# Kernel tuning notes

Measured on AMD Instinct MI355X. Metric: run time of the kernel, lower is better.

The kernel has to match this reference:

```python
import jax, jax.numpy as jnp
import numpy as np

B, H, W = 16, 512, 512
N_BINS = 511          # round(mean(shape)) - 1 for (512, 512)
MAX_R = 1.0           # (1 + min(shape)/max(shape)) / 2 for square image


def _bin_ids():
    # Precompute per-pixel radial shell index (replaces the list of boolean shell masks).
    frame = max(H, W)
    xx, yy = np.mgrid[:H, :W]
    ellipse = ((xx - H / 2) * 2 / frame) ** 2 + ((yy - W / 2) * 2 / frame) ** 2
    r2 = np.linspace(0.0, MAX_R, N_BINS + 1)[1:] ** 2
    # shell k = { r2[k-1] <= ellipse < r2[k] }; pixels with ellipse >= r2[-1] map to
    # overflow bin N_BINS and are dropped, exactly matching the xor'd ellipse masks.
    return jnp.asarray(np.searchsorted(r2, ellipse.ravel(), side='right').astype(np.int32))


BIN_IDS = _bin_ids()  # [H*W] int32 in [0, N_BINS]


def setup_inputs() -> dict:
    key = jax.random.key(0)
    k1, k2 = jax.random.split(key)
    return {
        "z_": jax.random.normal(k1, (B, H, W, 2), dtype=jnp.float32),
        "t_": jax.random.normal(k2, (B, H, W, 2), dtype=jnp.float32),
    }


def _shell_sums(x):
    # x: [B, H*W] -> per-shell sums [B, N_BINS+1] in a single fused segment-sum pass.
    return jax.vmap(lambda v: jax.ops.segment_sum(v, BIN_IDS, num_segments=N_BINS + 1))(x)


def reference(z_, t_):
    tc = t_[..., 0] + 1j * t_[..., 1]          # [B,H,W] complex target
    zc = z_[..., 0] + 1j * z_[..., 1]
    Ft = jnp.fft.fft2(tc, axes=(-2, -1))
    Fe = jnp.fft.fft2(zc - tc, axes=(-2, -1))
    norm_coeff = Ft.real ** 2 + Ft.imag ** 2   # |FFT(target)|^2, [B,H,W]
    errors = Fe.real ** 2 + Fe.imag ** 2       # |FFT(z - target)|^2
    es = _shell_sums(errors.reshape(B, -1))[:, :N_BINS]      # drop overflow bin
    ns = _shell_sums(norm_coeff.reshape(B, -1))[:, :N_BINS]
    nre = es / jnp.maximum(ns, 1e-8)           # per-batch, per-shell normed error
    # per_shell_loss = per-batch sum over shells; loss = mean over batch
    return jnp.mean(jnp.sum(nre, axis=1))
```

## Files before the change

kernel.cpp:

```cpp
#include <hip/hip_runtime.h>

#define HH 512
#define WW 512
#define NBATCH 16
#define NBINS 512

#define PI_F 3.14159265358979323846f

#define SW(r) ((r) ^ (((r) >> 4) & 0xF))

__device__ __forceinline__ float2 cadd(float2 a, float2 b){ return make_float2(a.x+b.x, a.y+b.y); }
__device__ __forceinline__ float2 csub(float2 a, float2 b){ return make_float2(a.x-b.x, a.y-b.y); }
__device__ __forceinline__ float2 cmul(float2 a, float2 b){
    return make_float2(a.x*b.x - a.y*b.y, a.x*b.y + a.y*b.x);
}

typedef __fp16 h2v __attribute__((ext_vector_type(2)));
__device__ __forceinline__ unsigned pack2(float2 v) {
    union { h2v h; unsigned u; } c;
    c.h = __builtin_amdgcn_cvt_pkrtz(v.x, v.y);
    return c.u;
}
__device__ __forceinline__ float2 unpack2(unsigned u) {
    union { unsigned u; __fp16 h[2]; } c; c.u = u;
    return make_float2((float)c.h[0], (float)c.h[1]);
}

__device__ __forceinline__ void dft8(const float2* a, float2* y) {
    const float s2 = 0.70710678118654752440f;
    float2 t02a = cadd(a[0], a[4]), t02s = csub(a[0], a[4]);
    float2 t13a = cadd(a[2], a[6]), t13s = csub(a[2], a[6]);
    float2 E0 = cadd(t02a, t13a);
    float2 E2 = csub(t02a, t13a);
    float2 E1 = make_float2(t02s.x + t13s.y, t02s.y - t13s.x);
    float2 E3 = make_float2(t02s.x - t13s.y, t02s.y + t13s.x);
    float2 u02a = cadd(a[1], a[5]), u02s = csub(a[1], a[5]);
    float2 u13a = cadd(a[3], a[7]), u13s = csub(a[3], a[7]);
    float2 O0 = cadd(u02a, u13a);
    float2 O2 = csub(u02a, u13a);
    float2 O1 = make_float2(u02s.x + u13s.y, u02s.y - u13s.x);
    float2 O3 = make_float2(u02s.x - u13s.y, u02s.y + u13s.x);
    float2 wO1 = make_float2(s2 * (O1.x + O1.y), s2 * (O1.y - O1.x));
    float2 wO2 = make_float2(O2.y, -O2.x);
    float2 wO3 = make_float2(s2 * (O3.y - O3.x), -s2 * (O3.x + O3.y));
    y[0] = cadd(E0, O0);  y[4] = csub(E0, O0);
    y[1] = cadd(E1, wO1); y[5] = csub(E1, wO1);
    y[2] = cadd(E2, wO2); y[6] = csub(E2, wO2);
    y[3] = cadd(E3, wO3); y[7] = csub(E3, wO3);
}

__device__ __forceinline__ void twiddle8(float base, float2* w) {
    float s1, c1, s4, c4;
    __sincosf(base, &s1, &c1);
    __sincosf(4.0f * base, &s4, &c4);
    w[0] = make_float2(1.0f, 0.0f);
    w[1] = make_float2(c1, s1);
    w[2] = cmul(w[1], w[1]);
    w[3] = cmul(w[2], w[1]);
    w[4] = make_float2(c4, s4);
    w[5] = cmul(w[4], w[1]);
    w[6] = cmul(w[4], w[2]);
    w[7] = cmul(w[4], w[3]);
}

__device__ __forceinline__ void fft512_x2(float2* rb0, float2* rb1, int lane,
                                          float2* a0, float2* a1,
                                          float2* y0, float2* y1) {
    float2 w[8], y[8];
    twiddle8(-PI_F * (float)lane * (1.0f / 256.0f), w);
    dft8(a0, y);
#pragma unroll
    for (int r = 0; r < 8; ++r) rb0[SW(8 * lane + r)] = cmul(y[r], w[r]);
    dft8(a1, y);
#pragma unroll
    for (int r = 0; r < 8; ++r) rb1[SW(8 * lane + r)] = cmul(y[r], w[r]);
    __builtin_amdgcn_wave_barrier();
#pragma unroll
    for (int u = 0; u < 8; ++u) a0[u] = rb0[SW(lane + 64 * u)];
#pragma unroll
    for (int u = 0; u < 8; ++u) a1[u] = rb1[SW(lane + 64 * u)];
    twiddle8(-PI_F * (float)(lane >> 3) * (1.0f / 32.0f), w);
    const int qb = (lane & 7) + ((lane >> 3) << 6);
    dft8(a0, y);
#pragma unroll
    for (int r = 0; r < 8; ++r) rb0[SW(qb + 8 * r)] = cmul(y[r], w[r]);
    dft8(a1, y);
#pragma unroll
    for (int r = 0; r < 8; ++r) rb1[SW(qb + 8 * r)] = cmul(y[r], w[r]);
    __builtin_amdgcn_wave_barrier();
#pragma unroll
    for (int u = 0; u < 8; ++u) a0[u] = rb0[SW(lane + 64 * u)];
#pragma unroll
    for (int u = 0; u < 8; ++u) a1[u] = rb1[SW(lane + 64 * u)];
    dft8(a0, y0);
    dft8(a1, y1);
}

__global__ __launch_bounds__(512, 4)
void row_fft_kernel(const float2* __restrict__ z, const float2* __restrict__ t,
                    unsigned* __restrict__ fieldsT) {
    __shared__ float2 buf[16 * 512];
    const int tid  = threadIdx.x;
    const int lane = tid & 63;
    const int g    = tid >> 6;
    const int bid  = blockIdx.x;
    const int hg   = bid & 31;
    const int b    = bid >> 5;
    const int hb   = hg << 4;
    const int r0   = hb | (g << 1);
    const size_t off0 = (((size_t)b * HH) + r0) << 9;
    const size_t off1 = off0 + 512;

    float2* rb0 = buf + ((g << 1) << 9);
    float2* rb1 = rb0 + 512;
    unsigned* tile = (unsigned*)buf;

#pragma unroll
    for (int f = 0; f < 2; ++f) {
        float2 a0[8], a1[8];
        if (f == 0) {
#pragma unroll
            for (int u = 0; u < 8; ++u) a0[u] = t[off0 + lane + 64 * u];
#pragma unroll
            for (int u = 0; u < 8; ++u) a1[u] = t[off1 + lane + 64 * u];
        } else {
#pragma unroll
            for (int u = 0; u < 8; ++u) {
                float2 zv = z[off0 + lane + 64 * u];
                float2 tv = t[off0 + lane + 64 * u];
                a0[u] = make_float2(zv.x - tv.x, zv.y - tv.y);
            }
#pragma unroll
            for (int u = 0; u < 8; ++u) {
                float2 zv = z[off1 + lane + 64 * u];
                float2 tv = t[off1 + lane + 64 * u];
                a1[u] = make_float2(zv.x - tv.x, zv.y - tv.y);
            }
        }
        float2 y0[8], y1[8];
        fft512_x2(rb0, rb1, lane, a0, a1, y0, y1);

        __syncthreads();
        const int rr0 = g << 1, rr1 = rr0 | 1;
#pragma unroll
        for (int r = 0; r < 8; ++r) {
            int c = lane + (r << 6);
            tile[rr0 * 516 + c] = pack2(y0[r]);
            tile[rr1 * 516 + c] = pack2(y1[r]);
        }
        __syncthreads();
        unsigned* outF = fieldsT + (((size_t)(b * 2 + f)) << 18);
#pragma unroll
        for (int k = 0; k < 4; ++k) {
            int e = tid + (k << 9);
            int c = e >> 2, q = e & 3;
            uint4 v;
            v.x = tile[(4 * q + 0) * 516 + c];
            v.y = tile[(4 * q + 1) * 516 + c];
            v.z = tile[(4 * q + 2) * 516 + c];
            v.w = tile[(4 * q + 3) * 516 + c];
            *(uint4*)(outF + (((size_t)c) << 9) + hb + (q << 2)) = v;
        }
        __syncthreads();
    }
}

__global__ __launch_bounds__(256, 4)
void col_fft_bin_kernel(const unsigned* __restrict__ fieldsT,
                        float* __restrict__ bins) {
    __shared__ float2 buf[8 * 512];
    __shared__ float hist[NBINS];
    const int tid  = threadIdx.x;
    const int lane = tid & 63;
    const int g    = tid >> 6;
    const int bid  = blockIdx.x;
    const int cg   = bid & 63;
    const int fl   = bid >> 6;
    const int f    = fl & 1;
    const int b    = fl >> 1;
    const int cA   = (cg << 3) | (g << 1);

    hist[tid] = 0.0f;
    hist[tid + 256] = 0.0f;
    __syncthreads();

    const unsigned* colA = fieldsT + ((((size_t)fl) << 9) + cA) * 512;
    const unsigned* colB = colA + 512;
    float2 a0[8], a1[8];
#pragma unroll
    for (int u = 0; u < 8; ++u) a0[u] = unpack2(colA[lane + (u << 6)]);
#pragma unroll
    for (int u = 0; u < 8; ++u) a1[u] = unpack2(colB[lane + (u << 6)]);

    float2* rb0 = buf + ((g << 1) << 9);
    float2* rb1 = rb0 + 512;
    float2 y0[8], y1[8];
    fft512_x2(rb0, rb1, lane, a0, a1, y0, y1);

    const float fcA = (float)(cA - 256)     * (1.0f / 256.0f);
    const float fcB = (float)(cA + 1 - 256) * (1.0f / 256.0f);
    const float fc2A = fcA * fcA, fc2B = fcB * fcB;
#pragma unroll
    for (int r = 0; r < 8; ++r) {
        int k = lane + (r << 6);
        float fr = (float)(k - 256) * (1.0f / 256.0f);
        float fr2 = fr * fr;
        float eA = fr2 + fc2A;
        float eB = fr2 + fc2B;
        if (eA < 1.0f) {
            int bin = (int)(sqrtf(eA) * 511.0f);
            atomicAdd(&hist[bin], y0[r].x * y0[r].x + y0[r].y * y0[r].y);
        }
        if (eB < 1.0f) {
            int bin = (int)(sqrtf(eB) * 511.0f);
            atomicAdd(&hist[bin], y1[r].x * y1[r].x + y1[r].y * y1[r].y);
        }
    }
    __syncthreads();
    float* gb = bins + ((size_t)f * NBATCH + b) * NBINS;
    atomicAdd(&gb[tid],       hist[tid]);
    atomicAdd(&gb[tid + 256], hist[tid + 256]);
}

__global__ __launch_bounds__(512)
void loss_kernel(const float* __restrict__ bins, float* __restrict__ outp) {
    __shared__ float red[512];
    const int tid = threadIdx.x;
    float acc = 0.0f;
    if (tid < 511) {
#pragma unroll 4
        for (int b = 0; b < NBATCH; ++b) {
            float ns = bins[((size_t)b) * NBINS + tid];
            float es = bins[((size_t)(NBATCH + b)) * NBINS + tid];
            acc += es / fmaxf(ns, 1e-8f);
        }
    }
    red[tid] = acc;
    __syncthreads();
    for (int s = 256; s > 0; s >>= 1) {
        if (tid < s) red[tid] += red[tid + s];
        __syncthreads();
    }
    if (tid == 0) outp[0] = red[0] * (1.0f / NBATCH);
}

extern "C" void kernel_launch(void* const* d_in, const int* in_sizes, int n_in,
                              void* d_out, int out_size, void* d_ws, size_t ws_size,
                              hipStream_t stream) {
    const float2* z = (const float2*)d_in[0];
    const float2* t = (const float2*)d_in[1];
    float* outp = (float*)d_out;

    const size_t binsBytes = (size_t)2 * NBATCH * NBINS * sizeof(float);
    float*    bins    = (float*)d_ws;
    unsigned* fieldsT = (unsigned*)((char*)d_ws + binsBytes);

    (void)hipMemsetAsync(bins, 0, binsBytes, stream);

    row_fft_kernel<<<NBATCH * 32, 512, 0, stream>>>(z, t, fieldsT);
    col_fft_bin_kernel<<<NBATCH * 2 * 64, 256, 0, stream>>>(fieldsT, bins);
    loss_kernel<<<1, 512, 0, stream>>>(bins, outp);
}
```

Before: 173.6 us.

## Interleave column pairs in transposed buffer, shrink row blocks, per-wave histograms

The row FFT kernel now uses 256-thread blocks handling 8 rows and loads t and z once up front, so t is not read twice. The intermediate transposed buffer is re-laid out so each column pair is stored interleaved. This lets the column kernel fetch both columns with a single 8-byte load per element. The column kernel replaces the shared block histogram with per-wave histograms that reuse the FFT scratch buffer, cutting atomic contention, and sums the four wave histograms before the global atomics. The tradeoff is more registers held live in the row kernel and smaller, 8-byte-granular transposed stores.

```diff
diff --git a/kernel.cpp b/kernel.cpp
--- a/kernel.cpp
+++ b/kernel.cpp
@@ -96,52 +96,54 @@
     dft8(a1, y1);
 }
 
-__global__ __launch_bounds__(512, 4)
+
+__global__ __launch_bounds__(256, 4)
 void row_fft_kernel(const float2* __restrict__ z, const float2* __restrict__ t,
                     unsigned* __restrict__ fieldsT) {
-    __shared__ float2 buf[16 * 512];
+    __shared__ float2 buf[8 * 512];
     const int tid  = threadIdx.x;
     const int lane = tid & 63;
     const int g    = tid >> 6;
     const int bid  = blockIdx.x;
-    const int hg   = bid & 31;
-    const int b    = bid >> 5;
-    const int hb   = hg << 4;
-    const int r0   = hb | (g << 1);
-    const size_t off0 = (((size_t)b * HH) + r0) << 9;
+    const int hg   = bid & 63;
+    const int b    = bid >> 6;
+    const int hb   = hg << 3;
+    const size_t off0 = (((size_t)b * HH) + hb + (g << 1)) << 9;
     const size_t off1 = off0 + 512;
+
+    float2 tv0[8], tv1[8], ev0[8], ev1[8];
+#pragma unroll
+    for (int u = 0; u < 8; ++u) tv0[u] = t[off0 + lane + 64 * u];
+#pragma unroll
+    for (int u = 0; u < 8; ++u) tv1[u] = t[off1 + lane + 64 * u];
+#pragma unroll
+    for (int u = 0; u < 8; ++u) {
+        float2 zv = z[off0 + lane + 64 * u];
+        ev0[u] = make_float2(zv.x - tv0[u].x, zv.y - tv0[u].y);
+    }
+#pragma unroll
+    for (int u = 0; u < 8; ++u) {
+        float2 zv = z[off1 + lane + 64 * u];
+        ev1[u] = make_float2(zv.x - tv1[u].x, zv.y - tv1[u].y);
+    }
 
     float2* rb0 = buf + ((g << 1) << 9);
     float2* rb1 = rb0 + 512;
     unsigned* tile = (unsigned*)buf;
+    const int rr0 = g << 1, rr1 = rr0 | 1;
 
 #pragma unroll
     for (int f = 0; f < 2; ++f) {
         float2 a0[8], a1[8];
-        if (f == 0) {
-#pragma unroll
-            for (int u = 0; u < 8; ++u) a0[u] = t[off0 + lane + 64 * u];
-#pragma unroll
-            for (int u = 0; u < 8; ++u) a1[u] = t[off1 + lane + 64 * u];
-        } else {
-#pragma unroll
-            for (int u = 0; u < 8; ++u) {
-                float2 zv = z[off0 + lane + 64 * u];
-                float2 tv = t[off0 + lane + 64 * u];
-                a0[u] = make_float2(zv.x - tv.x, zv.y - tv.y);
-            }
-#pragma unroll
-            for (int u = 0; u < 8; ++u) {
-                float2 zv = z[off1 + lane + 64 * u];
-                float2 tv = t[off1 + lane + 64 * u];
-                a1[u] = make_float2(zv.x - tv.x, zv.y - tv.y);
-            }
+#pragma unroll
+        for (int u = 0; u < 8; ++u) {
+            a0[u] = (f == 0) ? tv0[u] : ev0[u];
+            a1[u] = (f == 0) ? tv1[u] : ev1[u];
         }
         float2 y0[8], y1[8];
         fft512_x2(rb0, rb1, lane, a0, a1, y0, y1);
 
         __syncthreads();
-        const int rr0 = g << 1, rr1 = rr0 | 1;
 #pragma unroll
         for (int r = 0; r < 8; ++r) {
             int c = lane + (r << 6);
@@ -152,14 +154,14 @@
         unsigned* outF = fieldsT + (((size_t)(b * 2 + f)) << 18);
 #pragma unroll
         for (int k = 0; k < 4; ++k) {
-            int e = tid + (k << 9);
-            int c = e >> 2, q = e & 3;
+            int e  = tid + (k << 8);
+            int cp = e >> 2, q = e & 3;
             uint4 v;
-            v.x = tile[(4 * q + 0) * 516 + c];
-            v.y = tile[(4 * q + 1) * 516 + c];
-            v.z = tile[(4 * q + 2) * 516 + c];
-            v.w = tile[(4 * q + 3) * 516 + c];
-            *(uint4*)(outF + (((size_t)c) << 9) + hb + (q << 2)) = v;
+            v.x = tile[(2 * q)     * 516 + 2 * cp];
+            v.y = tile[(2 * q)     * 516 + 2 * cp + 1];
+            v.z = tile[(2 * q + 1) * 516 + 2 * cp];
+            v.w = tile[(2 * q + 1) * 516 + 2 * cp + 1];
+            *(uint4*)(outF + ((size_t)cp << 10) + ((hb + 2 * q) << 1)) = v;
         }
         __syncthreads();
     }
@@ -169,33 +171,36 @@
 void col_fft_bin_kernel(const unsigned* __restrict__ fieldsT,
                         float* __restrict__ bins) {
     __shared__ float2 buf[8 * 512];
-    __shared__ float hist[NBINS];
     const int tid  = threadIdx.x;
     const int lane = tid & 63;
     const int g    = tid >> 6;
     const int bid  = blockIdx.x;
-    const int cg   = bid & 63;
+    const int cgrp = bid & 63;
     const int fl   = bid >> 6;
     const int f    = fl & 1;
     const int b    = fl >> 1;
-    const int cA   = (cg << 3) | (g << 1);
-
-    hist[tid] = 0.0f;
-    hist[tid + 256] = 0.0f;
-    __syncthreads();
-
-    const unsigned* colA = fieldsT + ((((size_t)fl) << 9) + cA) * 512;
-    const unsigned* colB = colA + 512;
+    const int cp   = (cgrp << 2) | g;
+    const int cA   = cp << 1;
+
+    const uint2* colP = (const uint2*)(fieldsT + (((size_t)fl) << 18) + ((size_t)cp << 10));
     float2 a0[8], a1[8];
 #pragma unroll
-    for (int u = 0; u < 8; ++u) a0[u] = unpack2(colA[lane + (u << 6)]);
-#pragma unroll
-    for (int u = 0; u < 8; ++u) a1[u] = unpack2(colB[lane + (u << 6)]);
+    for (int u = 0; u < 8; ++u) {
+        uint2 v = colP[lane + (u << 6)];
+        a0[u] = unpack2(v.x);
+        a1[u] = unpack2(v.y);
+    }
 
     float2* rb0 = buf + ((g << 1) << 9);
     float2* rb1 = rb0 + 512;
     float2 y0[8], y1[8];
     fft512_x2(rb0, rb1, lane, a0, a1, y0, y1);
+    __builtin_amdgcn_wave_barrier();
+
+    float* Hw = (float*)rb0;
+#pragma unroll
+    for (int i = 0; i < 8; ++i) Hw[lane + (i << 6)] = 0.0f;
+    __builtin_amdgcn_wave_barrier();
 
     const float fcA = (float)(cA - 256)     * (1.0f / 256.0f);
     const float fcB = (float)(cA + 1 - 256) * (1.0f / 256.0f);
@@ -209,17 +214,23 @@
         float eB = fr2 + fc2B;
         if (eA < 1.0f) {
             int bin = (int)(sqrtf(eA) * 511.0f);
-            atomicAdd(&hist[bin], y0[r].x * y0[r].x + y0[r].y * y0[r].y);
+            atomicAdd(&Hw[bin], y0[r].x * y0[r].x + y0[r].y * y0[r].y);
         }
         if (eB < 1.0f) {
             int bin = (int)(sqrtf(eB) * 511.0f);
-            atomicAdd(&hist[bin], y1[r].x * y1[r].x + y1[r].y * y1[r].y);
+            atomicAdd(&Hw[bin], y1[r].x * y1[r].x + y1[r].y * y1[r].y);
         }
     }
     __syncthreads();
+
+    const float* H = (const float*)buf;
     float* gb = bins + ((size_t)f * NBATCH + b) * NBINS;
-    atomicAdd(&gb[tid],       hist[tid]);
-    atomicAdd(&gb[tid + 256], hist[tid + 256]);
+#pragma unroll
+    for (int j = 0; j < 2; ++j) {
+        int bin = tid + (j << 8);
+        float s = H[bin] + H[bin + 2048] + H[bin + 4096] + H[bin + 6144];
+        atomicAdd(&gb[bin], s);
+    }
 }
 
 __global__ __launch_bounds__(512)
@@ -257,7 +268,7 @@
 
     (void)hipMemsetAsync(bins, 0, binsBytes, stream);
 
-    row_fft_kernel<<<NBATCH * 32, 512, 0, stream>>>(z, t, fieldsT);
+    row_fft_kernel<<<NBATCH * 64, 256, 0, stream>>>(z, t, fieldsT);
     col_fft_bin_kernel<<<NBATCH * 2 * 64, 256, 0, stream>>>(fieldsT, bins);
     loss_kernel<<<1, 512, 0, stream>>>(bins, outp);
 }
```

Result: faster. 163.8 us (-5.6%).
